# Optimization experiments

Measured on AMD Instinct MI355X. Metric: run time of the kernel, lower is better.

The kernel has to match this reference:

```python
import jax, jax.numpy as jnp
import numpy as np


def setup_inputs() -> dict:
    key = jax.random.key(0)
    k1, k2, k3 = jax.random.split(key, 3)
    B, T, D, H = 256, 100, 4096, 1024
    # Xavier-uniform style init scales for the two parameter matrices
    zlim = float(np.sqrt(6.0 / (H + D)))
    klim = float(np.sqrt(6.0 / (D + H)))
    x = (jax.random.uniform(k1, (B, T, D), dtype=jnp.float32) < 0.1).astype(jnp.float32)  # sparse basket indicators
    Z = jax.random.uniform(k2, (H, D), dtype=jnp.float32, minval=-zlim, maxval=zlim)
    KFinv = jax.random.uniform(k3, (D, H), dtype=jnp.float32, minval=-klim, maxval=klim)
    b_out = jnp.zeros((D,), dtype=jnp.float32)
    b_hidden = jnp.zeros((H,), dtype=jnp.float32)
    return {"x": x, "Z": Z, "b_out": b_out, "KFinv": KFinv, "b_hidden": b_hidden}


def reference(x, Z, b_out, KFinv, b_hidden):
    # x: [B, T, D]; Z: [H, D]; KFinv: [D, H]
    B = x.shape[0]
    H = Z.shape[0]
    # initial hidden state is zeros -> initial next_basket = b_out (no sigmoid on step 0 prediction)
    h0 = jnp.zeros((H,), dtype=x.dtype)
    nb0 = jnp.broadcast_to(h0 @ Z + b_out, (B, Z.shape[1]))  # [B, D]

    def step(next_basket, xt):
        # xt: [B, D]
        diff = xt - next_basket                      # [B, D]
        hidden = diff @ KFinv + b_hidden             # [B, H]
        nb = jax.nn.sigmoid(hidden @ Z + b_out)      # [B, D]
        return nb, nb

    xs = jnp.swapaxes(x, 0, 1)                       # [T, B, D]
    _, preds = jax.lax.scan(step, nb0, xs)           # preds: [T, B, D]
    return jnp.swapaxes(preds, 0, 1)                 # [B, T, D]
```

## Files before the change

### kernel.cpp

```cpp
#include <hip/hip_runtime.h>
#include <hip/hip_cooperative_groups.h>

#define T_SEQ 100
#define DD 4096
#define HH 1024
#define BB 256

#define GRID_WG 256
#define BLOCK_T 512

typedef __attribute__((ext_vector_type(8))) short short8;
typedef __attribute__((ext_vector_type(4))) float float4_t;

__device__ __forceinline__ short f2bf(float f) {
  union { float f; unsigned u; } v; v.f = f;
  unsigned r = v.u + 0x7fffu + ((v.u >> 16) & 1u);
  return (short)(r >> 16);
}

__global__ __launch_bounds__(256) void transpose_cvt(const float* __restrict__ src,
                                                     short* __restrict__ dst,
                                                     int K, int N) {
  __shared__ float tile[32][33];
  int k0 = blockIdx.x * 32, n0 = blockIdx.y * 32;
  int tx = threadIdx.x & 31, ty = threadIdx.x >> 5;
#pragma unroll
  for (int i = 0; i < 32; i += 8)
    tile[ty + i][tx] = src[(size_t)(k0 + ty + i) * N + n0 + tx];
  __syncthreads();
#pragma unroll
  for (int i = 0; i < 32; i += 8)
    dst[(size_t)(n0 + ty + i) * K + k0 + tx] = f2bf(tile[tx][ty + i]);
}

__global__ __launch_bounds__(BLOCK_T, 2) void gru_persist(
    const float* __restrict__ x, const short* __restrict__ KFt ,
    const short* __restrict__ Zt , const float* __restrict__ b_out,
    const float* __restrict__ b_hidden, short* __restrict__ diff ,
    float* __restrict__ hb , float* __restrict__ out) {
  __shared__ short smem[2][8704];
  auto grid = cooperative_groups::this_grid();

  const int g = blockIdx.x, tid = threadIdx.x;
  const int lane = tid & 63, wid = tid >> 6;
  const int quad = lane >> 4, l15 = lane & 15;
  const int gsize = GRID_WG * BLOCK_T;
  const int gtid = g * BLOCK_T + tid;

  for (int idx = gtid; idx < BB * DD; idx += gsize) {
    int m = idx >> 12, d = idx & (DD - 1);
    diff[idx] = f2bf(x[(size_t)m * T_SEQ * DD + d] - b_out[d]);
  }
  grid.sync();

  const int xcd = g & 7, loc = g >> 3;
  const int maA = (loc & 7) * 32;
  const int naA = (4 * xcd + (loc >> 3)) * 32;
  const int wkA = wid >> 2, wqA = wid & 3;
  const int wmA = wqA >> 1, wnA = wqA & 1;
  const int maB = (loc & 3) * 64;
  const int naB = (8 * xcd + (loc >> 2)) * 64;
  const int wmB = wid >> 1, wnB = wid & 1;
  const int srA = tid >> 4, scA = tid & 15;
  const int srB = tid >> 3, scB = tid & 7;

  for (int t = 0; t < T_SEQ; ++t) {
    {
      float4_t acc = {0.f, 0.f, 0.f, 0.f};
      short* sA = smem[0];
      short* sB = smem[1];
#pragma unroll 1
      for (int it = 0; it < 16; ++it) {
        const int kb = it * 256;
        const short* gp = &diff[(size_t)(maA + srA) * DD + kb + scA * 16];
        short8 v0 = *(const short8*)gp;
        short8 v1 = *(const short8*)(gp + 8);
        const short* gq = &KFt[(size_t)(naA + srA) * DD + kb + scA * 16];
        short8 u0 = *(const short8*)gq;
        short8 u1 = *(const short8*)(gq + 8);
        *(short8*)&sA[srA * 264 + scA * 16] = v0;
        *(short8*)&sA[srA * 264 + scA * 16 + 8] = v1;
        *(short8*)&sB[srA * 264 + scA * 16] = u0;
        *(short8*)&sB[srA * 264 + scA * 16 + 8] = u1;
        __syncthreads();
        const int ko = wkA * 128;
#pragma unroll
        for (int ks = 0; ks < 4; ++ks) {
          short8 a = *(const short8*)&sA[(wmA * 16 + l15) * 264 + ko + ks * 32 + quad * 8];
          short8 b = *(const short8*)&sB[(wnA * 16 + l15) * 264 + ko + ks * 32 + quad * 8];
          acc = __builtin_amdgcn_mfma_f32_16x16x32_bf16(a, b, acc, 0, 0, 0);
        }
        __syncthreads();
      }
      float* red = (float*)smem[0];
      if (wkA == 1) {
#pragma unroll
        for (int r = 0; r < 4; ++r) red[(wqA * 64 + lane) * 4 + r] = acc[r];
      }
      __syncthreads();
      if (wkA == 0) {
#pragma unroll
        for (int r = 0; r < 4; ++r) {
          float v = acc[r] + red[(wqA * 64 + lane) * 4 + r];
          int m = maA + wmA * 16 + quad * 4 + r;
          int n = naA + wnA * 16 + l15;
          hb[m * HH + n] = v + b_hidden[n];
        }
      }
    }
    grid.sync();

    {
      float4_t acc2[2] = {};
#pragma unroll 1
      for (int it = 0; it < 8; ++it) {
        const int kb = it * 128;
        const float* hp = &hb[(maB + srB) * HH + kb + scB * 16];
        short8 v0, v1;
#pragma unroll
        for (int j = 0; j < 8; ++j) v0[j] = f2bf(hp[j]);
#pragma unroll
        for (int j = 0; j < 8; ++j) v1[j] = f2bf(hp[8 + j]);
        const short* gq = &Zt[(size_t)(naB + srB) * HH + kb + scB * 16];
        short8 u0 = *(const short8*)gq;
        short8 u1 = *(const short8*)(gq + 8);
        *(short8*)&smem[0][srB * 136 + scB * 16] = v0;
        *(short8*)&smem[0][srB * 136 + scB * 16 + 8] = v1;
        *(short8*)&smem[1][srB * 136 + scB * 16] = u0;
        *(short8*)&smem[1][srB * 136 + scB * 16 + 8] = u1;
        __syncthreads();
#pragma unroll
        for (int ks = 0; ks < 4; ++ks) {
          short8 a  = *(const short8*)&smem[0][(wmB * 16 + l15) * 136 + ks * 32 + quad * 8];
          short8 b0 = *(const short8*)&smem[1][(wnB * 32 + l15) * 136 + ks * 32 + quad * 8];
          short8 b1 = *(const short8*)&smem[1][(wnB * 32 + 16 + l15) * 136 + ks * 32 + quad * 8];
          acc2[0] = __builtin_amdgcn_mfma_f32_16x16x32_bf16(a, b0, acc2[0], 0, 0, 0);
          acc2[1] = __builtin_amdgcn_mfma_f32_16x16x32_bf16(a, b1, acc2[1], 0, 0, 0);
        }
        __syncthreads();
      }
#pragma unroll
      for (int f = 0; f < 2; ++f)
#pragma unroll
        for (int r = 0; r < 4; ++r) {
          int m = maB + wmB * 16 + quad * 4 + r;
          int n = naB + wnB * 32 + f * 16 + l15;
          float z = acc2[f][r] + b_out[n];
          float s = 1.f / (1.f + __expf(-z));
          out[((size_t)m * T_SEQ + t) * DD + n] = s;
          if (t < T_SEQ - 1)
            diff[(size_t)m * DD + n] = f2bf(x[((size_t)m * T_SEQ + t + 1) * DD + n] - s);
        }
    }
    grid.sync();
  }
}

extern "C" void kernel_launch(void* const* d_in, const int* in_sizes, int n_in,
                              void* d_out, int out_size, void* d_ws, size_t ws_size,
                              hipStream_t stream) {
  const float* x = (const float*)d_in[0];
  const float* Z = (const float*)d_in[1];
  const float* b_out = (const float*)d_in[2];
  const float* KFinv = (const float*)d_in[3];
  const float* b_hidden = (const float*)d_in[4];
  float* out = (float*)d_out;

  char* ws = (char*)d_ws;
  short* KFt = (short*)ws;
  short* Zt = (short*)(ws + 8388608);
  short* diff = (short*)(ws + 16777216);
  float* hb = (float*)(ws + 18874368);

  transpose_cvt<<<dim3(128, 32), 256, 0, stream>>>(KFinv, KFt, 4096, 1024);
  transpose_cvt<<<dim3(32, 128), 256, 0, stream>>>(Z, Zt, 1024, 4096);

  void* args[] = {(void*)&x,        (void*)&KFt,  (void*)&Zt, (void*)&b_out,
                  (void*)&b_hidden, (void*)&diff, (void*)&hb, (void*)&out};
  hipLaunchCooperativeKernel((void*)gru_persist, dim3(GRID_WG), dim3(BLOCK_T), args, 0,
                             stream);
}
```

Measured before the change: 9.829 ms.

## Double-buffer LDS tiles with register prefetch, swizzle, and store hidden state as bf16

Both GEMM phases now use double-buffered LDS with register prefetch of the next K tile, so each iteration needs one barrier instead of two and global loads overlap the MFMA work. LDS rows use an XOR swizzle in place of padding to avoid bank conflicts. The hidden buffer is stored in bf16 instead of fp32, which halves its traffic and removes the per-element conversion in phase B. Weight tiles and next-step x values are prefetched before the grid syncs, and diff and hb writes are packed in pairs through lane shuffles. The cost is higher register pressure and more complex indexing.

```diff
diff --git a/kernel.cpp b/kernel.cpp
--- a/kernel.cpp
+++ b/kernel.cpp
@@ -16,6 +16,10 @@
   union { float f; unsigned u; } v; v.f = f;
   unsigned r = v.u + 0x7fffu + ((v.u >> 16) & 1u);
   return (short)(r >> 16);
+}
+
+__device__ __forceinline__ int swz(int row, int col) {
+  return col ^ ((row & 7) << 3);
 }
 
 __global__ __launch_bounds__(256) void transpose_cvt(const float* __restrict__ src,
@@ -37,8 +41,8 @@
     const float* __restrict__ x, const short* __restrict__ KFt ,
     const short* __restrict__ Zt , const float* __restrict__ b_out,
     const float* __restrict__ b_hidden, short* __restrict__ diff ,
-    float* __restrict__ hb , float* __restrict__ out) {
-  __shared__ short smem[2][8704];
+    short* __restrict__ hb , float* __restrict__ out) {
+  __shared__ short smem[2][2][8192];
   auto grid = cooperative_groups::this_grid();
 
   const int g = blockIdx.x, tid = threadIdx.x;
@@ -47,11 +51,13 @@
   const int gsize = GRID_WG * BLOCK_T;
   const int gtid = g * BLOCK_T + tid;
 
-  for (int idx = gtid; idx < BB * DD; idx += gsize) {
-    int m = idx >> 12, d = idx & (DD - 1);
-    diff[idx] = f2bf(x[(size_t)m * T_SEQ * DD + d] - b_out[d]);
+  for (int idx = gtid; idx < BB * DD / 2; idx += gsize) {
+    int m = idx >> 11, d = (idx & 2047) * 2;
+    const float* xp = &x[(size_t)m * T_SEQ * DD + d];
+    unsigned lo = (unsigned short)f2bf(xp[0] - b_out[d]);
+    unsigned hi = (unsigned short)f2bf(xp[1] - b_out[d + 1]);
+    ((unsigned*)diff)[idx] = lo | (hi << 16);
   }
-  grid.sync();
 
   const int xcd = g & 7, loc = g >> 3;
   const int maA = (loc & 7) * 32;
@@ -64,35 +70,60 @@
   const int srA = tid >> 4, scA = tid & 15;
   const int srB = tid >> 3, scB = tid & 7;
 
+  short8 wK[2], wD[2], wZ[2], wH[2];
+
+#pragma unroll
+  for (int j = 0; j < 2; ++j)
+    wK[j] = *(const short8*)&KFt[(size_t)(naA + srA) * DD + scA * 8 + j * 128];
+
+  grid.sync();
+
   for (int t = 0; t < T_SEQ; ++t) {
     {
       float4_t acc = {0.f, 0.f, 0.f, 0.f};
-      short* sA = smem[0];
-      short* sB = smem[1];
+#pragma unroll
+      for (int j = 0; j < 2; ++j)
+        wD[j] = *(const short8*)&diff[(size_t)(maA + srA) * DD + scA * 8 + j * 128];
+#pragma unroll
+      for (int j = 0; j < 2; ++j) {
+        int co = swz(srA, scA * 8 + j * 128);
+        *(short8*)&smem[0][0][srA * 256 + co] = wD[j];
+        *(short8*)&smem[0][1][srA * 256 + co] = wK[j];
+      }
+      int cur = 0;
+      const int arow = wmA * 16 + l15, brow = wnA * 16 + l15;
+      const int ko = wkA * 128;
 #pragma unroll 1
       for (int it = 0; it < 16; ++it) {
-        const int kb = it * 256;
-        const short* gp = &diff[(size_t)(maA + srA) * DD + kb + scA * 16];
-        short8 v0 = *(const short8*)gp;
-        short8 v1 = *(const short8*)(gp + 8);
-        const short* gq = &KFt[(size_t)(naA + srA) * DD + kb + scA * 16];
-        short8 u0 = *(const short8*)gq;
-        short8 u1 = *(const short8*)(gq + 8);
-        *(short8*)&sA[srA * 264 + scA * 16] = v0;
-        *(short8*)&sA[srA * 264 + scA * 16 + 8] = v1;
-        *(short8*)&sB[srA * 264 + scA * 16] = u0;
-        *(short8*)&sB[srA * 264 + scA * 16 + 8] = u1;
         __syncthreads();
-        const int ko = wkA * 128;
+        if (it < 15) {
+          const int kb = (it + 1) * 256;
+#pragma unroll
+          for (int j = 0; j < 2; ++j) {
+            wD[j] = *(const short8*)&diff[(size_t)(maA + srA) * DD + kb + scA * 8 + j * 128];
+            wK[j] = *(const short8*)&KFt[(size_t)(naA + srA) * DD + kb + scA * 8 + j * 128];
+          }
+        }
+        const short* sA = smem[cur][0];
+        const short* sB = smem[cur][1];
 #pragma unroll
         for (int ks = 0; ks < 4; ++ks) {
-          short8 a = *(const short8*)&sA[(wmA * 16 + l15) * 264 + ko + ks * 32 + quad * 8];
-          short8 b = *(const short8*)&sB[(wnA * 16 + l15) * 264 + ko + ks * 32 + quad * 8];
+          short8 a = *(const short8*)&sA[arow * 256 + swz(arow, ko + ks * 32 + quad * 8)];
+          short8 b = *(const short8*)&sB[brow * 256 + swz(brow, ko + ks * 32 + quad * 8)];
           acc = __builtin_amdgcn_mfma_f32_16x16x32_bf16(a, b, acc, 0, 0, 0);
         }
-        __syncthreads();
-      }
-      float* red = (float*)smem[0];
+        if (it < 15) {
+          cur ^= 1;
+#pragma unroll
+          for (int j = 0; j < 2; ++j) {
+            int co = swz(srA, scA * 8 + j * 128);
+            *(short8*)&smem[cur][0][srA * 256 + co] = wD[j];
+            *(short8*)&smem[cur][1][srA * 256 + co] = wK[j];
+          }
+        }
+      }
+      __syncthreads();
+      float* red = (float*)&smem[0][0][0];
       if (wkA == 1) {
 #pragma unroll
         for (int r = 0; r < 4; ++r) red[(wqA * 64 + lane) * 4 + r] = acc[r];
@@ -104,40 +135,76 @@
           float v = acc[r] + red[(wqA * 64 + lane) * 4 + r];
           int m = maA + wmA * 16 + quad * 4 + r;
           int n = naA + wnA * 16 + l15;
-          hb[m * HH + n] = v + b_hidden[n];
+          float hv = v + b_hidden[n];
+          float ov = __shfl_xor(hv, 1);
+          if (!(lane & 1)) {
+            unsigned w = (unsigned)(unsigned short)f2bf(hv) |
+                         ((unsigned)(unsigned short)f2bf(ov) << 16);
+            *(unsigned*)&hb[m * HH + n] = w;
+          }
         }
       }
     }
+#pragma unroll
+    for (int j = 0; j < 2; ++j)
+      wZ[j] = *(const short8*)&Zt[(size_t)(naB + srB) * HH + scB * 8 + j * 64];
     grid.sync();
 
     {
       float4_t acc2[2] = {};
+      float xr[8];
+      if (t < T_SEQ - 1) {
+#pragma unroll
+        for (int f = 0; f < 2; ++f)
+#pragma unroll
+          for (int r = 0; r < 4; ++r) {
+            int m = maB + wmB * 16 + quad * 4 + r;
+            int n = naB + wnB * 32 + f * 16 + l15;
+            xr[f * 4 + r] = x[((size_t)m * T_SEQ + t + 1) * DD + n];
+          }
+      }
+#pragma unroll
+      for (int j = 0; j < 2; ++j)
+        wH[j] = *(const short8*)&hb[(size_t)(maB + srB) * HH + scB * 8 + j * 64];
+#pragma unroll
+      for (int j = 0; j < 2; ++j) {
+        int co = swz(srB, scB * 8 + j * 64);
+        *(short8*)&smem[0][0][srB * 128 + co] = wH[j];
+        *(short8*)&smem[0][1][srB * 128 + co] = wZ[j];
+      }
+      int cur = 0;
+      const int arowB = wmB * 16 + l15;
+      const int b0row = wnB * 32 + l15, b1row = wnB * 32 + 16 + l15;
 #pragma unroll 1
       for (int it = 0; it < 8; ++it) {
-        const int kb = it * 128;
-        const float* hp = &hb[(maB + srB) * HH + kb + scB * 16];
-        short8 v0, v1;
-#pragma unroll
-        for (int j = 0; j < 8; ++j) v0[j] = f2bf(hp[j]);
-#pragma unroll
-        for (int j = 0; j < 8; ++j) v1[j] = f2bf(hp[8 + j]);
-        const short* gq = &Zt[(size_t)(naB + srB) * HH + kb + scB * 16];
-        short8 u0 = *(const short8*)gq;
-        short8 u1 = *(const short8*)(gq + 8);
-        *(short8*)&smem[0][srB * 136 + scB * 16] = v0;
-        *(short8*)&smem[0][srB * 136 + scB * 16 + 8] = v1;
-        *(short8*)&smem[1][srB * 136 + scB * 16] = u0;
-        *(short8*)&smem[1][srB * 136 + scB * 16 + 8] = u1;
         __syncthreads();
+        if (it < 7) {
+          const int kb = (it + 1) * 128;
+#pragma unroll
+          for (int j = 0; j < 2; ++j) {
+            wH[j] = *(const short8*)&hb[(size_t)(maB + srB) * HH + kb + scB * 8 + j * 64];
+            wZ[j] = *(const short8*)&Zt[(size_t)(naB + srB) * HH + kb + scB * 8 + j * 64];
+          }
+        }
+        const short* sA = smem[cur][0];
+        const short* sB = smem[cur][1];
 #pragma unroll
         for (int ks = 0; ks < 4; ++ks) {
-          short8 a  = *(const short8*)&smem[0][(wmB * 16 + l15) * 136 + ks * 32 + quad * 8];
-          short8 b0 = *(const short8*)&smem[1][(wnB * 32 + l15) * 136 + ks * 32 + quad * 8];
-          short8 b1 = *(const short8*)&smem[1][(wnB * 32 + 16 + l15) * 136 + ks * 32 + quad * 8];
+          short8 a  = *(const short8*)&sA[arowB * 128 + swz(arowB, ks * 32 + quad * 8)];
+          short8 b0 = *(const short8*)&sB[b0row * 128 + swz(b0row, ks * 32 + quad * 8)];
+          short8 b1 = *(const short8*)&sB[b1row * 128 + swz(b1row, ks * 32 + quad * 8)];
           acc2[0] = __builtin_amdgcn_mfma_f32_16x16x32_bf16(a, b0, acc2[0], 0, 0, 0);
           acc2[1] = __builtin_amdgcn_mfma_f32_16x16x32_bf16(a, b1, acc2[1], 0, 0, 0);
         }
-        __syncthreads();
+        if (it < 7) {
+          cur ^= 1;
+#pragma unroll
+          for (int j = 0; j < 2; ++j) {
+            int co = swz(srB, scB * 8 + j * 64);
+            *(short8*)&smem[cur][0][srB * 128 + co] = wH[j];
+            *(short8*)&smem[cur][1][srB * 128 + co] = wZ[j];
+          }
+        }
       }
 #pragma unroll
       for (int f = 0; f < 2; ++f)
@@ -148,9 +215,20 @@
           float z = acc2[f][r] + b_out[n];
           float s = 1.f / (1.f + __expf(-z));
           out[((size_t)m * T_SEQ + t) * DD + n] = s;
-          if (t < T_SEQ - 1)
-            diff[(size_t)m * DD + n] = f2bf(x[((size_t)m * T_SEQ + t + 1) * DD + n] - s);
-        }
+          if (t < T_SEQ - 1) {
+            short db = f2bf(xr[f * 4 + r] - s);
+            int ob = __shfl_xor((int)(unsigned short)db, 1);
+            if (!(lane & 1)) {
+              unsigned w = (unsigned)(unsigned short)db | ((unsigned)ob << 16);
+              *(unsigned*)&diff[(size_t)m * DD + n] = w;
+            }
+          }
+        }
+    }
+    if (t < T_SEQ - 1) {
+#pragma unroll
+      for (int j = 0; j < 2; ++j)
+        wK[j] = *(const short8*)&KFt[(size_t)(naA + srA) * DD + scA * 8 + j * 128];
     }
     grid.sync();
   }
@@ -170,7 +248,7 @@
   short* KFt = (short*)ws;
   short* Zt = (short*)(ws + 8388608);
   short* diff = (short*)(ws + 16777216);
-  float* hb = (float*)(ws + 18874368);
+  short* hb = (short*)(ws + 18874368);
 
   transpose_cvt<<<dim3(128, 32), 256, 0, stream>>>(KFinv, KFt, 4096, 1024);
   transpose_cvt<<<dim3(32, 128), 256, 0, stream>>>(Z, Zt, 1024, 4096);
```

New measurement: 8.666 ms. 11.8% less time.
